# Performance work log

Measured on AMD Instinct MI355X. Metric: run time of the kernel, lower is better.

The kernel has to match this reference:

```python
import jax, jax.numpy as jnp
import numpy as np

V, E, L, H, B, T = 32000, 1024, 6, 16, 4, 1024
HS = E // H
FF = 4 * E


def setup_inputs() -> dict:
    key = jax.random.key(0)
    ks = jax.random.split(key, 16)
    s = 0.02
    n = lambda k, shp: jax.random.normal(k, shp, jnp.float32) * s
    return {
        "tokens": jax.random.randint(ks[0], (B, T), 0, V),
        "tok_emb": n(ks[1], (V, E)),
        "pos_emb": n(ks[2], (T, E)),
        "Wq": n(ks[3], (L, E, E)),
        "Wk": n(ks[4], (L, E, E)),
        "Wv": n(ks[5], (L, E, E)),
        "Wo": n(ks[6], (L, E, E)),
        "ln1_g": jnp.ones((L, E), jnp.float32),
        "ln1_b": jnp.zeros((L, E), jnp.float32),
        "W1": n(ks[7], (L, E, FF)),
        "b1": jnp.zeros((L, FF), jnp.float32),
        "W2": n(ks[8], (L, FF, E)),
        "b2": jnp.zeros((L, E), jnp.float32),
        "ln2_g": jnp.ones((L, E), jnp.float32),
        "ln2_b": jnp.zeros((L, E), jnp.float32),
        "lmh_w": n(ks[9], (E, V)),
        "lmh_b": jnp.zeros((V,), jnp.float32),
    }


def _layernorm(x, g, b):
    m = jnp.mean(x, axis=-1, keepdims=True)
    v = jnp.var(x, axis=-1, keepdims=True)
    return (x - m) * jax.lax.rsqrt(v + 1e-5) * g + b


def _forward(tokens, tok_emb, pos_emb, Wq, Wk, Wv, Wo, ln1_g, ln1_b,
             W1, b1, W2, b2, ln2_g, ln2_b, lmh_w, lmh_b):
    Bb, Tt = tokens.shape
    x = tok_emb[tokens] + pos_emb[:Tt]  # [B,T,E]
    mask = jnp.tril(jnp.ones((Tt, Tt), bool))  # causal
    scale = jnp.float32(E) ** -0.5  # NOTE: original scales by emb_dim, not head_size

    def block(x, p):
        wq, wk, wv, wo, g1, be1, w1, bb1, w2, bb2, g2, be2 = p
        h = _layernorm(x, g1, be1)
        q = (h @ wq).reshape(Bb, Tt, H, HS)
        k = (h @ wk).reshape(Bb, Tt, H, HS)
        v = (h @ wv).reshape(Bb, Tt, H, HS)
        scores = jnp.einsum('bqhd,bkhd->bhqk', q, k) * scale
        scores = jnp.where(mask, scores, -jnp.inf)
        w = jax.nn.softmax(scores, axis=-1)
        attn = jnp.einsum('bhqk,bkhd->bqhd', w, v).reshape(Bb, Tt, E)
        x = x + attn @ wo
        h2 = _layernorm(x, g2, be2)
        x = x + jax.nn.relu(h2 @ w1 + bb1) @ w2 + bb2
        return x, None

    x, _ = jax.lax.scan(block, x, (Wq, Wk, Wv, Wo, ln1_g, ln1_b,
                                   W1, b1, W2, b2, ln2_g, ln2_b))
    logits = x @ lmh_w + lmh_b  # [B,T,V]
    return logits


def reference(tokens, tok_emb, pos_emb, Wq, Wk, Wv, Wo, ln1_g, ln1_b,
              W1, b1, W2, b2, ln2_g, ln2_b, lmh_w, lmh_b):
    return _forward(tokens, tok_emb, pos_emb, Wq, Wk, Wv, Wo, ln1_g, ln1_b,
                    W1, b1, W2, b2, ln2_g, ln2_b, lmh_w, lmh_b)
```

## Files before the change

### kernel.cpp

```cpp
#include <hip/hip_runtime.h>
#include <cstdint>
#include <cstddef>

typedef __bf16 bf16;
typedef __attribute__((ext_vector_type(8))) __bf16 bf16x8;
typedef __attribute__((ext_vector_type(4))) float f32x4;

constexpr int kV = 32000, kE = 1024, kL = 6, kH = 16, kB = 4, kT = 1024;
constexpr int kHS = 64, kFF = 4096;
constexpr int kM = kB * kT;
constexpr float kScale = 0.03125f;

typedef __attribute__((address_space(1))) void gv_t;
typedef __attribute__((address_space(3))) void lv_t;

__device__ inline void gload_lds16(const void* g, void* l) {
  __builtin_amdgcn_global_load_lds((gv_t*)g, (lv_t*)l, 16, 0, 0);
}

#define SB0() __builtin_amdgcn_sched_barrier(0)
#define LGK0() asm volatile("s_waitcnt lgkmcnt(0)" ::: "memory")

enum { EPI_BF16 = 0, EPI_BF16_BIAS_RELU = 1, EPI_F32 = 2, EPI_F32_RES = 3, EPI_F32_BIAS = 4 };

__device__ inline void xcd_swz(int& bx, int& by) {
  int gx = gridDim.x, gy = gridDim.y;
  int nxy = gx * gy;
  int orig = by * gx + bx;
  int q = nxy >> 3, r = nxy & 7, xcd = orig & 7, idx = orig >> 3;
  int logical = (xcd < r ? xcd * (q + 1) : r * (q + 1) + (xcd - r) * q) + idx;
  bx = logical / gy;
  by = logical % gy;
}

template <int EPI>
__global__ __launch_bounds__(512, 2) void gemm256_k(
    const bf16* __restrict__ Ag, const bf16* __restrict__ Bg, void* Cg,
    const float* __restrict__ bias, const float* __restrict__ resid,
    int K, long lda, long ldb, long ldc) {
  extern __shared__ bf16 lds[];
  constexpr int SL = 8192;
  bf16* As = lds;
  bf16* Bs = lds + 4 * SL;

  const int tid = threadIdx.x, lane = tid & 63, w = tid >> 6;
  int bx = blockIdx.x, by = blockIdx.y;
  xcd_swz(bx, by);
  const long tm = (long)by * 256, tn = (long)bx * 256;
  const int wr = w >> 2, wc = w & 3;
  const int lr = lane & 15, kg = lane >> 4;

  const int p0 = tid, p1 = 512 + tid;
  const int r0 = p0 >> 2, ls0 = (p0 & 3) ^ ((r0 >> 1) & 3);
  const int r1 = p1 >> 2, ls1 = (p1 & 3) ^ ((r1 >> 1) & 3);
  const bf16* a0 = Ag + (tm + r0) * lda + ls0 * 8;
  const bf16* a1 = Ag + (tm + r1) * lda + ls1 * 8;
  const bf16* b0 = Bg + (tn + r0) * ldb + ls0 * 8;
  const bf16* b1 = Bg + (tn + r1) * ldb + ls1 * 8;
  const int wb = w * 1024;

  auto stage = [&](int s) {
    const int slot = s & 3;
    const long k0 = (long)s * 32;
    char* Ab = (char*)As + slot * (SL * 2);
    char* Bb = (char*)Bs + slot * (SL * 2);
    gload_lds16(a0 + k0, Ab + wb);
    gload_lds16(a1 + k0, Ab + 8192 + wb);
    gload_lds16(b0 + k0, Bb + wb);
    gload_lds16(b1 + k0, Bb + 8192 + wb);
  };

  int aoff[8], boff[4];
#pragma unroll
  for (int mi = 0; mi < 8; mi++) {
    int ar = wr * 128 + mi * 16 + lr;
    aoff[mi] = ar * 64 + ((kg ^ ((ar >> 1) & 3)) << 4);
  }
#pragma unroll
  for (int ni = 0; ni < 4; ni++) {
    int br = wc * 64 + ni * 16 + lr;
    boff[ni] = br * 64 + ((kg ^ ((br >> 1) & 3)) << 4);
  }

  f32x4 acc[8][4] = {};
  stage(0);
  stage(1);
  stage(2);
  const int NS = K >> 5;
  for (int s = 0; s < NS; s++) {
    SB0();
    if (s <= NS - 3)
      asm volatile("s_waitcnt vmcnt(8)" ::: "memory");
    else if (s == NS - 2)
      asm volatile("s_waitcnt vmcnt(4)" ::: "memory");
    else
      asm volatile("s_waitcnt vmcnt(0)" ::: "memory");
    __builtin_amdgcn_s_barrier();
    SB0();
    if (s + 3 < NS) stage(s + 3);
    const char* Ab = (const char*)As + (s & 3) * (SL * 2);
    const char* Bb = (const char*)Bs + (s & 3) * (SL * 2);
    bf16x8 af[8], bfr[4];
#pragma unroll
    for (int mi = 0; mi < 8; mi++) af[mi] = *(const bf16x8*)(Ab + aoff[mi]);
#pragma unroll
    for (int ni = 0; ni < 4; ni++) bfr[ni] = *(const bf16x8*)(Bb + boff[ni]);
    __builtin_amdgcn_s_setprio(1);
#pragma unroll
    for (int mi = 0; mi < 8; mi++)
#pragma unroll
      for (int ni = 0; ni < 4; ni++)
        acc[mi][ni] =
            __builtin_amdgcn_mfma_f32_16x16x32_bf16(af[mi], bfr[ni], acc[mi][ni], 0, 0, 0);
    __builtin_amdgcn_s_setprio(0);
  }

#pragma unroll
  for (int mi = 0; mi < 8; mi++) {
#pragma unroll
    for (int ni = 0; ni < 4; ni++) {
      const long rr = tm + wr * 128 + mi * 16 + kg * 4;
      const long cc = tn + wc * 64 + ni * 16 + lr;
      float bi = 0.f;
      if constexpr (EPI == EPI_BF16_BIAS_RELU || EPI == EPI_F32_BIAS) bi = bias[cc];
      if constexpr (EPI == EPI_F32_RES) bi = bias ? bias[cc] : 0.f;
#pragma unroll
      for (int j = 0; j < 4; j++) {
        long off = (rr + j) * ldc + cc;
        float val = acc[mi][ni][j];
        if constexpr (EPI == EPI_BF16)
          ((bf16*)Cg)[off] = (bf16)val;
        else if constexpr (EPI == EPI_BF16_BIAS_RELU)
          ((bf16*)Cg)[off] = (bf16)fmaxf(val + bi, 0.f);
        else if constexpr (EPI == EPI_F32)
          ((float*)Cg)[off] = val;
        else if constexpr (EPI == EPI_F32_RES)
          ((float*)Cg)[off] = resid[off] + val + bi;
        else
          ((float*)Cg)[off] = val + bi;
      }
    }
  }
}

template <int EPI>
__global__ __launch_bounds__(256, 2) void ring128_k(
    const bf16* __restrict__ Ag, const bf16* __restrict__ Bg, void* Cg,
    const float* __restrict__ bias, const float* __restrict__ resid,
    int K, long lda, long ldb, long ldc) {
  extern __shared__ bf16 lds[];
  char* Lb = (char*)lds;
  const int tid = threadIdx.x, lane = tid & 63, w = tid >> 6;
  int bx = blockIdx.x, by = blockIdx.y;
  xcd_swz(bx, by);
  const long tm = (long)by * 128, tn = (long)bx * 128;
  const int wr = w >> 1, wc = w & 1;
  const int lr = lane & 15, kg = lane >> 4;

  const int r0 = tid >> 2, g0 = (tid & 3) ^ ((r0 >> 1) & 3);
  const int r1 = (256 + tid) >> 2, g1 = ((256 + tid) & 3) ^ ((r1 >> 1) & 3);
  const bf16* a0 = Ag + (tm + r0) * lda + g0 * 8;
  const bf16* a1 = Ag + (tm + r1) * lda + g1 * 8;
  const bf16* b0 = Bg + (tn + r0) * ldb + g0 * 8;
  const bf16* b1 = Bg + (tn + r1) * ldb + g1 * 8;
  const int wb = w * 1024;

  auto stage = [&](int s) {
    const int slot = s & 3;
    const long k0 = (long)s * 32;
    char* Ab = Lb + slot * 16384;
    char* Bb = Ab + 8192;
    gload_lds16(a0 + k0, Ab + wb);
    gload_lds16(a1 + k0, Ab + 4096 + wb);
    gload_lds16(b0 + k0, Bb + wb);
    gload_lds16(b1 + k0, Bb + 4096 + wb);
  };

  int aoff[4], boff[4];
#pragma unroll
  for (int mi = 0; mi < 4; mi++) {
    int ar = wr * 64 + mi * 16 + lr;
    aoff[mi] = ar * 64 + ((kg ^ ((ar >> 1) & 3)) << 4);
  }
#pragma unroll
  for (int ni = 0; ni < 4; ni++) {
    int br = wc * 64 + ni * 16 + lr;
    boff[ni] = br * 64 + ((kg ^ ((br >> 1) & 3)) << 4);
  }

  f32x4 acc[4][4] = {};
  stage(0);
  stage(1);
  stage(2);
  const int NS = K >> 5;
  for (int s = 0; s < NS; s++) {
    SB0();
    if (s <= NS - 3)
      asm volatile("s_waitcnt vmcnt(8)" ::: "memory");
    else if (s == NS - 2)
      asm volatile("s_waitcnt vmcnt(4)" ::: "memory");
    else
      asm volatile("s_waitcnt vmcnt(0)" ::: "memory");
    __builtin_amdgcn_s_barrier();
    SB0();
    if (s + 3 < NS) stage(s + 3);
    const char* Ab = Lb + (s & 3) * 16384;
    const char* Bb = Ab + 8192;
    bf16x8 af[4], bfr[4];
#pragma unroll
    for (int mi = 0; mi < 4; mi++) af[mi] = *(const bf16x8*)(Ab + aoff[mi]);
#pragma unroll
    for (int ni = 0; ni < 4; ni++) bfr[ni] = *(const bf16x8*)(Bb + boff[ni]);
    __builtin_amdgcn_s_setprio(1);
#pragma unroll
    for (int mi = 0; mi < 4; mi++)
#pragma unroll
      for (int ni = 0; ni < 4; ni++)
        acc[mi][ni] =
            __builtin_amdgcn_mfma_f32_16x16x32_bf16(af[mi], bfr[ni], acc[mi][ni], 0, 0, 0);
    __builtin_amdgcn_s_setprio(0);
  }

#pragma unroll
  for (int mi = 0; mi < 4; mi++) {
#pragma unroll
    for (int ni = 0; ni < 4; ni++) {
      const long rr = tm + wr * 64 + mi * 16 + kg * 4;
      const long cc = tn + wc * 64 + ni * 16 + lr;
      float bi = 0.f;
      if constexpr (EPI == EPI_BF16_BIAS_RELU || EPI == EPI_F32_BIAS) bi = bias[cc];
      if constexpr (EPI == EPI_F32_RES) bi = bias ? bias[cc] : 0.f;
#pragma unroll
      for (int j = 0; j < 4; j++) {
        long off = (rr + j) * ldc + cc;
        float val = acc[mi][ni][j];
        if constexpr (EPI == EPI_BF16)
          ((bf16*)Cg)[off] = (bf16)val;
        else if constexpr (EPI == EPI_BF16_BIAS_RELU)
          ((bf16*)Cg)[off] = (bf16)fmaxf(val + bi, 0.f);
        else if constexpr (EPI == EPI_F32)
          ((float*)Cg)[off] = val;
        else if constexpr (EPI == EPI_F32_RES)
          ((float*)Cg)[off] = resid[off] + val + bi;
        else
          ((float*)Cg)[off] = val + bi;
      }
    }
  }
}

template <int BM, int BN, int WM, int WN, int EPI, bool CAUSAL>
__global__ __launch_bounds__((BM / WM) * (BN / WN) * 64) void gemm_k(
    const bf16* __restrict__ Ag, const bf16* __restrict__ Bg, void* Cg,
    const float* __restrict__ bias, const float* resid, int K, long lda, long ldb,
    long ldc, long sA1, long sA2, long sB1, long sB2, long sC1, long sC2, int zdiv) {
  constexpr int BK = 32;
  constexpr int NWM = BM / WM, NWN = BN / WN, NW = NWM * NWN, THREADS = NW * 64;
  constexpr int MI = WM / 16, NI = WN / 16;
  constexpr int A_CH = (BM * BK * 2) / (THREADS * 16);
  constexpr int B_CH = (BN * BK * 2) / (THREADS * 16);
  static_assert(A_CH >= 1 && B_CH >= 1, "staging chunks");
  __shared__ bf16 As[2][BM * BK];
  __shared__ bf16 Bs[2][BN * BK];
  const int tid = threadIdx.x, lane = tid & 63;
  int bx = blockIdx.x, by = blockIdx.y;
  const int z = blockIdx.z;
  if (gridDim.z == 1) xcd_swz(bx, by);
  const long tm = (long)by * BM, tn = (long)bx * BN;
  if (CAUSAL && tn > tm + (BM - 1)) return;
  const int zq = z / zdiv, zr = z % zdiv;
  Ag += (long)zq * sA1 + (long)zr * sA2;
  Bg += (long)zq * sB1 + (long)zr * sB2;
  const long cbase = (long)zq * sC1 + (long)zr * sC2;
  const int w = tid >> 6;
  const int wr = w / NWN, wc = w % NWN;
  const int wm0 = wr * WM, wn0 = wc * WN;
  const int lr = lane & 15, kg = lane >> 4;
  f32x4 acc[MI][NI] = {};

  auto stage = [&](int buf, int k0) {
#pragma unroll
    for (int i = 0; i < A_CH; i++) {
      int qq = i * THREADS + tid;
      gload_lds16(Ag + (tm + (qq >> 2)) * lda + k0 + (qq & 3) * 8,
                  (char*)&As[buf][0] + (i * THREADS + (tid & ~63)) * 16);
    }
#pragma unroll
    for (int i = 0; i < B_CH; i++) {
      int qq = i * THREADS + tid;
      gload_lds16(Bg + (tn + (qq >> 2)) * ldb + k0 + (qq & 3) * 8,
                  (char*)&Bs[buf][0] + (i * THREADS + (tid & ~63)) * 16);
    }
  };

  const int nt = K / BK;
  stage(0, 0);
  __syncthreads();
  int cur = 0;
  for (int t = 0; t < nt; t++) {
    if (t + 1 < nt) stage(cur ^ 1, (t + 1) * BK);
    bf16x8 af[MI], bfr[NI];
#pragma unroll
    for (int mi = 0; mi < MI; mi++)
      af[mi] = *(const bf16x8*)&As[cur][(wm0 + mi * 16 + lr) * BK + kg * 8];
#pragma unroll
    for (int ni = 0; ni < NI; ni++)
      bfr[ni] = *(const bf16x8*)&Bs[cur][(wn0 + ni * 16 + lr) * BK + kg * 8];
#pragma unroll
    for (int mi = 0; mi < MI; mi++)
#pragma unroll
      for (int ni = 0; ni < NI; ni++)
        acc[mi][ni] =
            __builtin_amdgcn_mfma_f32_16x16x32_bf16(af[mi], bfr[ni], acc[mi][ni], 0, 0, 0);
    __syncthreads();
    cur ^= 1;
  }

#pragma unroll
  for (int mi = 0; mi < MI; mi++) {
#pragma unroll
    for (int ni = 0; ni < NI; ni++) {
      const long rr = tm + wm0 + mi * 16 + kg * 4;
      const long cc = tn + wn0 + ni * 16 + lr;
      float bi = 0.f;
      if constexpr (EPI == EPI_BF16_BIAS_RELU || EPI == EPI_F32_BIAS) bi = bias[cc];
      if constexpr (EPI == EPI_F32_RES) bi = bias ? bias[cc] : 0.f;
#pragma unroll
      for (int j = 0; j < 4; j++) {
        long off = cbase + (rr + j) * ldc + cc;
        float val = acc[mi][ni][j];
        if constexpr (EPI == EPI_BF16)
          ((bf16*)Cg)[off] = (bf16)val;
        else if constexpr (EPI == EPI_BF16_BIAS_RELU)
          ((bf16*)Cg)[off] = (bf16)fmaxf(val + bi, 0.f);
        else if constexpr (EPI == EPI_F32)
          ((float*)Cg)[off] = val;
        else if constexpr (EPI == EPI_F32_RES)
          ((float*)Cg)[off] = resid[off] + val + bi;
        else
          ((float*)Cg)[off] = val + bi;
      }
    }
  }
}

__global__ __launch_bounds__(256, 2) void fa_k(const bf16* __restrict__ qkv,
                                               bf16* __restrict__ out) {
  extern __shared__ bf16 lds[];
  char* L = (char*)lds;
  const int tid = threadIdx.x, lane = tid & 63, wq = tid >> 6;
  const int lr = lane & 15, kg = lane >> 4;
  const int pair = blockIdx.x, z = blockIdx.y;
  const int b = z >> 4, hh = z & 15;
  const long bq = (long)b * kT;

  auto stageKV = [&](int buf, int t) {
    const bf16* kb = qkv + (bq + t * 64) * 3072 + 1024 + hh * 64;
#pragma unroll
    for (int i = 0; i < 2; i++) {
      int p = i * 256 + tid;
      int key = p >> 3, s = p & 7;
      gload_lds16(kb + (long)key * 3072 + ((s ^ (key & 7)) * 8),
                  L + 16384 + buf * 8192 + (i * 256 + (tid & ~63)) * 16);
      gload_lds16(kb + (long)key * 3072 + 1024 + s * 8,
                  L + 32768 + buf * 8192 + (i * 256 + (tid & ~63)) * 16);
    }
  };
  char* Pw = L + 58368 + wq * 4608;

  for (int sidx = 0; sidx < 2; sidx++) {
    const int qt = sidx ? 7 - pair : pair;
    const int q0 = qt * 128;
    const bf16* qbase = qkv + (bq + q0) * 3072 + hh * 64;

#pragma unroll
    for (int i = 0; i < 4; i++) {
      int p = i * 256 + tid;
      int row = p >> 3, s = p & 7;
      gload_lds16(qbase + (long)row * 3072 + ((s ^ (row & 7)) * 8),
                  L + (i * 256 + (tid & ~63)) * 16);
    }
    stageKV(0, 0);
    __syncthreads();

    bf16x8 qf[2][2];
#pragma unroll
    for (int mi = 0; mi < 2; mi++)
#pragma unroll
      for (int ks = 0; ks < 2; ks++) {
        int qr = wq * 32 + mi * 16 + lr;
        qf[mi][ks] = *(const bf16x8*)(L + qr * 128 + ((ks * 64 + kg * 16) ^ ((qr & 7) << 4)));
      }

    f32x4 O[2][4] = {};
    float mrun[2][4], lrun[2][4];
#pragma unroll
    for (int mi = 0; mi < 2; mi++)
#pragma unroll
      for (int j = 0; j < 4; j++) {
        mrun[mi][j] = -3e38f;
        lrun[mi][j] = 0.f;
      }

    const int nt = 2 * qt + 2;
    int cur = 0;
    for (int t = 0; t < nt; t++) {
      if (t + 1 < nt) stageKV(cur ^ 1, t + 1);
      {
        const char* Vb = L + 32768 + cur * 8192;
        char* VTb = L + 49152;
#pragma unroll
        for (int i = 0; i < 2; i++) {
          int p = i * 256 + tid;
          int key = p >> 3, s = p & 7;
          bf16x8 vv = *(const bf16x8*)(Vb + p * 16);
#pragma unroll
          for (int e = 0; e < 8; e++)
            *(bf16*)(VTb + (s * 8 + e) * 144 + ((key * 2) ^ (s << 4))) = vv[e];
        }
      }
      LGK0();
      SB0();
      __builtin_amdgcn_s_barrier();
      SB0();

      const char* Kb = L + 16384 + cur * 8192;
      f32x4 S[2][4] = {};
#pragma unroll
      for (int ks = 0; ks < 2; ks++) {
        bf16x8 kf[4];
#pragma unroll
        for (int ni = 0; ni < 4; ni++) {
          int key = ni * 16 + lr;
          kf[ni] = *(const bf16x8*)(Kb + key * 128 + ((ks * 64 + kg * 16) ^ ((key & 7) << 4)));
        }
#pragma unroll
        for (int mi = 0; mi < 2; mi++)
#pragma unroll
          for (int ni = 0; ni < 4; ni++)
            S[mi][ni] =
                __builtin_amdgcn_mfma_f32_16x16x32_bf16(qf[mi][ks], kf[ni], S[mi][ni], 0, 0, 0);
      }

      const int kv0 = t * 64;
#pragma unroll
      for (int mi = 0; mi < 2; mi++) {
        const int qg = q0 + wq * 32 + mi * 16 + kg * 4;
#pragma unroll
        for (int j = 0; j < 4; j++) {
          float m0 = -3e38f;
#pragma unroll
          for (int ni = 0; ni < 4; ni++) {
            float v = (kv0 + ni * 16 + lr > qg + j) ? -3e38f : S[mi][ni][j];
            S[mi][ni][j] = v;
            m0 = fmaxf(m0, v);
          }
          m0 = fmaxf(m0, __shfl_xor(m0, 1));
          m0 = fmaxf(m0, __shfl_xor(m0, 2));
          m0 = fmaxf(m0, __shfl_xor(m0, 4));
          m0 = fmaxf(m0, __shfl_xor(m0, 8));
          float mnew = fmaxf(mrun[mi][j], m0);
          float alpha = __expf((mrun[mi][j] - mnew) * kScale);
          mrun[mi][j] = mnew;
          lrun[mi][j] *= alpha;
#pragma unroll
          for (int di = 0; di < 4; di++) O[mi][di][j] *= alpha;
          float rs = 0.f;
#pragma unroll
          for (int ni = 0; ni < 4; ni++) {
            float v = S[mi][ni][j];
            float p = (v <= -1e38f) ? 0.f : __expf((v - mnew) * kScale);
            S[mi][ni][j] = p;
            rs += p;
          }
          rs += __shfl_xor(rs, 1);
          rs += __shfl_xor(rs, 2);
          rs += __shfl_xor(rs, 4);
          rs += __shfl_xor(rs, 8);
          lrun[mi][j] += rs;
        }
#pragma unroll
        for (int ni = 0; ni < 4; ni++)
#pragma unroll
          for (int j = 0; j < 4; j++)
            *(bf16*)(Pw + (mi * 16 + kg * 4 + j) * 144 + (ni * 16 + lr) * 2) =
                (bf16)S[mi][ni][j];
      }
      LGK0();
      SB0();

      const char* VTb = L + 49152;
#pragma unroll
      for (int ks = 0; ks < 2; ks++) {
        bf16x8 pf[2], vf[4];
#pragma unroll
        for (int mi = 0; mi < 2; mi++)
          pf[mi] = *(const bf16x8*)(Pw + (mi * 16 + lr) * 144 + ks * 64 + kg * 16);
#pragma unroll
        for (int di = 0; di < 4; di++) {
          int d = di * 16 + lr;
          vf[di] =
              *(const bf16x8*)(VTb + d * 144 + ((ks * 64 + kg * 16) ^ (((d >> 3) & 7) << 4)));
        }
#pragma unroll
        for (int mi = 0; mi < 2; mi++)
#pragma unroll
          for (int di = 0; di < 4; di++)
            O[mi][di] =
                __builtin_amdgcn_mfma_f32_16x16x32_bf16(pf[mi], vf[di], O[mi][di], 0, 0, 0);
      }
      __syncthreads();
      cur ^= 1;
    }

#pragma unroll
    for (int mi = 0; mi < 2; mi++)
#pragma unroll
      for (int j = 0; j < 4; j++) {
        float inv = 1.f / lrun[mi][j];
        long grow = bq + q0 + wq * 32 + mi * 16 + kg * 4 + j;
#pragma unroll
        for (int di = 0; di < 4; di++)
          out[grow * kE + hh * 64 + di * 16 + lr] = (bf16)(O[mi][di][j] * inv);
      }
  }
}

__global__ void tcvt_k(const float* __restrict__ in, bf16* __restrict__ out, int K, int N,
                       long in_zs, long out_zs) {
  __shared__ float t[32][33];
  long z = blockIdx.z;
  in += z * in_zs;
  out += z * out_zs;
  int n0 = blockIdx.x * 32, k0 = blockIdx.y * 32;
  int tx = threadIdx.x, ty = threadIdx.y;
#pragma unroll
  for (int i = 0; i < 32; i += 8) t[ty + i][tx] = in[(long)(k0 + ty + i) * N + n0 + tx];
  __syncthreads();
#pragma unroll
  for (int i = 0; i < 32; i += 8)
    out[(long)(n0 + ty + i) * K + k0 + tx] = (bf16)t[tx][ty + i];
}

__global__ void embed_k(const int* __restrict__ toks, const float* __restrict__ te,
                        const float* __restrict__ pe, float* __restrict__ x) {
  int row = blockIdx.x, tid = threadIdx.x;
  int t = row & (kT - 1);
  long tok = toks[row];
  float4 a = ((const float4*)(te + tok * kE))[tid];
  float4 p = ((const float4*)(pe + (long)t * kE))[tid];
  float4 r{a.x + p.x, a.y + p.y, a.z + p.z, a.w + p.w};
  ((float4*)(x + (long)row * kE))[tid] = r;
}

__global__ void ln_k(const float* __restrict__ x, const float* __restrict__ g,
                     const float* __restrict__ b, bf16* __restrict__ h) {
  int row = blockIdx.x, tid = threadIdx.x, lane = tid & 63, w = tid >> 6;
  const float4 v = ((const float4*)(x + (long)row * kE))[tid];
  float s = v.x + v.y + v.z + v.w;
  float ss = v.x * v.x + v.y * v.y + v.z * v.z + v.w * v.w;
#pragma unroll
  for (int o = 32; o; o >>= 1) {
    s += __shfl_xor(s, o);
    ss += __shfl_xor(ss, o);
  }
  __shared__ float r1[4], r2[4];
  if (lane == 0) { r1[w] = s; r2[w] = ss; }
  __syncthreads();
  s = r1[0] + r1[1] + r1[2] + r1[3];
  ss = r2[0] + r2[1] + r2[2] + r2[3];
  float mean = s * (1.f / kE);
  float var = ss * (1.f / kE) - mean * mean;
  float rs = rsqrtf(var + 1e-5f);
  float4 gg = ((const float4*)g)[tid];
  float4 bb = ((const float4*)b)[tid];
  union { bf16 o[4]; uint2 u; } pk;
  pk.o[0] = (bf16)((v.x - mean) * rs * gg.x + bb.x);
  pk.o[1] = (bf16)((v.y - mean) * rs * gg.y + bb.y);
  pk.o[2] = (bf16)((v.z - mean) * rs * gg.z + bb.z);
  pk.o[3] = (bf16)((v.w - mean) * rs * gg.w + bb.w);
  ((uint2*)(h + (long)row * kE))[tid] = pk.u;
}

__global__ void cast_k(const float* __restrict__ x, bf16* __restrict__ o) {
  long i = (long)blockIdx.x * 256 + threadIdx.x;
  float4 v = ((const float4*)x)[i];
  union { bf16 b[4]; uint2 u; } pk;
  pk.b[0] = (bf16)v.x;
  pk.b[1] = (bf16)v.y;
  pk.b[2] = (bf16)v.z;
  pk.b[3] = (bf16)v.w;
  ((uint2*)o)[i] = pk.u;
}

extern "C" void kernel_launch(void* const* d_in, const int* in_sizes, int n_in,
                              void* d_out, int out_size, void* d_ws, size_t ws_size,
                              hipStream_t stream) {
  const int* toks = (const int*)d_in[0];
  const float* te = (const float*)d_in[1];
  const float* pe = (const float*)d_in[2];
  const float* Wq = (const float*)d_in[3];
  const float* Wk = (const float*)d_in[4];
  const float* Wv = (const float*)d_in[5];
  const float* Wo = (const float*)d_in[6];
  const float* g1 = (const float*)d_in[7];
  const float* be1 = (const float*)d_in[8];
  const float* W1 = (const float*)d_in[9];
  const float* bb1 = (const float*)d_in[10];
  const float* W2 = (const float*)d_in[11];
  const float* bb2 = (const float*)d_in[12];
  const float* g2 = (const float*)d_in[13];
  const float* be2 = (const float*)d_in[14];
  const float* lmw = (const float*)d_in[15];
  const float* lmb = (const float*)d_in[16];

  hipFuncSetAttribute(reinterpret_cast<const void*>(&gemm256_k<EPI_BF16>),
                      hipFuncAttributeMaxDynamicSharedMemorySize, 131072);
  hipFuncSetAttribute(reinterpret_cast<const void*>(&gemm256_k<EPI_BF16_BIAS_RELU>),
                      hipFuncAttributeMaxDynamicSharedMemorySize, 131072);
  hipFuncSetAttribute(reinterpret_cast<const void*>(&gemm256_k<EPI_F32_BIAS>),
                      hipFuncAttributeMaxDynamicSharedMemorySize, 131072);
  hipFuncSetAttribute(reinterpret_cast<const void*>(&ring128_k<EPI_F32_RES>),
                      hipFuncAttributeMaxDynamicSharedMemorySize, 65536);
  hipFuncSetAttribute(reinterpret_cast<const void*>(&fa_k),
                      hipFuncAttributeMaxDynamicSharedMemorySize, 76800);

  char* ws = (char*)d_ws;
  size_t off = 0;
  auto alloc = [&](size_t bytes) -> char* {
    char* p = ws + off;
    off += (bytes + 255) & ~(size_t)255;
    return p;
  };
  bf16* WqkvT = (bf16*)alloc((size_t)kL * 3 * kE * kE * 2);
  bf16* WoT = (bf16*)alloc((size_t)kL * kE * kE * 2);
  bf16* W1T = (bf16*)alloc((size_t)kL * kE * kFF * 2);
  bf16* W2T = (bf16*)alloc((size_t)kL * kE * kFF * 2);
  bf16* lmT = (bf16*)alloc((size_t)kV * kE * 2);
  float* x = (float*)alloc((size_t)kM * kE * 4);
  bf16* h = (bf16*)alloc((size_t)kM * kE * 2);
  bf16* qkv = (bf16*)alloc((size_t)kM * 3 * kE * 2);
  bf16* at = (bf16*)alloc((size_t)kM * kE * 2);

  bf16* mid = (bf16*)d_out;

  const long EE = (long)kE * kE;
  dim3 tb(32, 8);
  tcvt_k<<<dim3(kE / 32, kE / 32, kL), tb, 0, stream>>>(Wq, WqkvT, kE, kE, EE, 3 * EE);
  tcvt_k<<<dim3(kE / 32, kE / 32, kL), tb, 0, stream>>>(Wk, WqkvT + EE, kE, kE, EE, 3 * EE);
  tcvt_k<<<dim3(kE / 32, kE / 32, kL), tb, 0, stream>>>(Wv, WqkvT + 2 * EE, kE, kE, EE, 3 * EE);
  tcvt_k<<<dim3(kE / 32, kE / 32, kL), tb, 0, stream>>>(Wo, WoT, kE, kE, EE, EE);
  tcvt_k<<<dim3(kFF / 32, kE / 32, kL), tb, 0, stream>>>(W1, W1T, kE, kFF, 4 * EE, 4 * EE);
  tcvt_k<<<dim3(kE / 32, kFF / 32, kL), tb, 0, stream>>>(W2, W2T, kFF, kE, 4 * EE, 4 * EE);
  tcvt_k<<<dim3(kV / 32, kE / 32, 1), tb, 0, stream>>>(lmw, lmT, kE, kV, 0, 0);

  embed_k<<<kM, 256, 0, stream>>>(toks, te, pe, x);

  for (int l = 0; l < kL; l++) {
    ln_k<<<kM, 256, 0, stream>>>(x, g1 + l * kE, be1 + l * kE, h);
    gemm256_k<EPI_BF16><<<dim3(3 * kE / 256, kM / 256), 512, 131072, stream>>>(
        h, WqkvT + (size_t)l * 3 * EE, qkv, nullptr, nullptr, kE, kE, kE, 3 * kE);
    fa_k<<<dim3(4, kB * kH), 256, 76800, stream>>>(qkv, at);
    gemm_k<128, 128, 64, 64, EPI_F32_RES, false><<<dim3(kE / 128, kM / 128, 1), 256, 0, stream>>>(
        at, WoT + (size_t)l * EE, x, nullptr, x, kE, kE, kE, kE, 0, 0, 0, 0, 0, 0, 1);
    ln_k<<<kM, 256, 0, stream>>>(x, g2 + l * kE, be2 + l * kE, h);
    gemm256_k<EPI_BF16_BIAS_RELU><<<dim3(kFF / 256, kM / 256), 512, 131072, stream>>>(
        h, W1T + (size_t)l * (size_t)kFF * kE, mid, bb1 + l * kFF, nullptr, kE, kE, kE, kFF);
    ring128_k<EPI_F32_RES><<<dim3(kE / 128, kM / 128), 256, 65536, stream>>>(
        mid, W2T + (size_t)l * (size_t)kE * kFF, x, bb2 + l * kE, x, kFF, kFF, kFF, kE);
  }
  cast_k<<<kM * kE / 1024, 256, 0, stream>>>(x, h);
  gemm256_k<EPI_F32_BIAS><<<dim3(kV / 256, kM / 256), 512, 131072, stream>>>(
      h, lmT, d_out, lmb, nullptr, kE, kE, kE, kV);
}
```

Before: 2.122 ms.

## Pre-transpose V globally and split flash-attention grid per query tile

```diff
diff --git a/kernel.cpp b/kernel.cpp
--- a/kernel.cpp
+++ b/kernel.cpp
@@ -249,280 +249,186 @@
   }
 }
 
-template <int BM, int BN, int WM, int WN, int EPI, bool CAUSAL>
-__global__ __launch_bounds__((BM / WM) * (BN / WN) * 64) void gemm_k(
-    const bf16* __restrict__ Ag, const bf16* __restrict__ Bg, void* Cg,
-    const float* __restrict__ bias, const float* resid, int K, long lda, long ldb,
-    long ldc, long sA1, long sA2, long sB1, long sB2, long sC1, long sC2, int zdiv) {
-  constexpr int BK = 32;
-  constexpr int NWM = BM / WM, NWN = BN / WN, NW = NWM * NWN, THREADS = NW * 64;
-  constexpr int MI = WM / 16, NI = WN / 16;
-  constexpr int A_CH = (BM * BK * 2) / (THREADS * 16);
-  constexpr int B_CH = (BN * BK * 2) / (THREADS * 16);
-  static_assert(A_CH >= 1 && B_CH >= 1, "staging chunks");
-  __shared__ bf16 As[2][BM * BK];
-  __shared__ bf16 Bs[2][BN * BK];
-  const int tid = threadIdx.x, lane = tid & 63;
-  int bx = blockIdx.x, by = blockIdx.y;
-  const int z = blockIdx.z;
-  if (gridDim.z == 1) xcd_swz(bx, by);
-  const long tm = (long)by * BM, tn = (long)bx * BN;
-  if (CAUSAL && tn > tm + (BM - 1)) return;
-  const int zq = z / zdiv, zr = z % zdiv;
-  Ag += (long)zq * sA1 + (long)zr * sA2;
-  Bg += (long)zq * sB1 + (long)zr * sB2;
-  const long cbase = (long)zq * sC1 + (long)zr * sC2;
-  const int w = tid >> 6;
-  const int wr = w / NWN, wc = w % NWN;
-  const int wm0 = wr * WM, wn0 = wc * WN;
-  const int lr = lane & 15, kg = lane >> 4;
-  f32x4 acc[MI][NI] = {};
-
-  auto stage = [&](int buf, int k0) {
-#pragma unroll
-    for (int i = 0; i < A_CH; i++) {
-      int qq = i * THREADS + tid;
-      gload_lds16(Ag + (tm + (qq >> 2)) * lda + k0 + (qq & 3) * 8,
-                  (char*)&As[buf][0] + (i * THREADS + (tid & ~63)) * 16);
-    }
-#pragma unroll
-    for (int i = 0; i < B_CH; i++) {
-      int qq = i * THREADS + tid;
-      gload_lds16(Bg + (tn + (qq >> 2)) * ldb + k0 + (qq & 3) * 8,
-                  (char*)&Bs[buf][0] + (i * THREADS + (tid & ~63)) * 16);
-    }
-  };
-
-  const int nt = K / BK;
-  stage(0, 0);
-  __syncthreads();
-  int cur = 0;
-  for (int t = 0; t < nt; t++) {
-    if (t + 1 < nt) stage(cur ^ 1, (t + 1) * BK);
-    bf16x8 af[MI], bfr[NI];
-#pragma unroll
-    for (int mi = 0; mi < MI; mi++)
-      af[mi] = *(const bf16x8*)&As[cur][(wm0 + mi * 16 + lr) * BK + kg * 8];
-#pragma unroll
-    for (int ni = 0; ni < NI; ni++)
-      bfr[ni] = *(const bf16x8*)&Bs[cur][(wn0 + ni * 16 + lr) * BK + kg * 8];
-#pragma unroll
-    for (int mi = 0; mi < MI; mi++)
-#pragma unroll
-      for (int ni = 0; ni < NI; ni++)
-        acc[mi][ni] =
-            __builtin_amdgcn_mfma_f32_16x16x32_bf16(af[mi], bfr[ni], acc[mi][ni], 0, 0, 0);
-    __syncthreads();
-    cur ^= 1;
-  }
-
-#pragma unroll
-  for (int mi = 0; mi < MI; mi++) {
-#pragma unroll
-    for (int ni = 0; ni < NI; ni++) {
-      const long rr = tm + wm0 + mi * 16 + kg * 4;
-      const long cc = tn + wn0 + ni * 16 + lr;
-      float bi = 0.f;
-      if constexpr (EPI == EPI_BF16_BIAS_RELU || EPI == EPI_F32_BIAS) bi = bias[cc];
-      if constexpr (EPI == EPI_F32_RES) bi = bias ? bias[cc] : 0.f;
-#pragma unroll
-      for (int j = 0; j < 4; j++) {
-        long off = cbase + (rr + j) * ldc + cc;
-        float val = acc[mi][ni][j];
-        if constexpr (EPI == EPI_BF16)
-          ((bf16*)Cg)[off] = (bf16)val;
-        else if constexpr (EPI == EPI_BF16_BIAS_RELU)
-          ((bf16*)Cg)[off] = (bf16)fmaxf(val + bi, 0.f);
-        else if constexpr (EPI == EPI_F32)
-          ((float*)Cg)[off] = val;
-        else if constexpr (EPI == EPI_F32_RES)
-          ((float*)Cg)[off] = resid[off] + val + bi;
-        else
-          ((float*)Cg)[off] = val + bi;
-      }
-    }
-  }
-}
-
 __global__ __launch_bounds__(256, 2) void fa_k(const bf16* __restrict__ qkv,
+                                               const bf16* __restrict__ vtG,
                                                bf16* __restrict__ out) {
   extern __shared__ bf16 lds[];
   char* L = (char*)lds;
   const int tid = threadIdx.x, lane = tid & 63, wq = tid >> 6;
   const int lr = lane & 15, kg = lane >> 4;
-  const int pair = blockIdx.x, z = blockIdx.y;
-  const int b = z >> 4, hh = z & 15;
+  const int bh = blockIdx.x, z = blockIdx.y;
+  const int b = bh >> 4, hh = bh & 15;
   const long bq = (long)b * kT;
-
+  const int qt = z < 4 ? z : 11 - z;
+  const int q0 = qt * 128;
+  const bf16* qbase = qkv + (bq + q0) * 3072 + hh * 64;
+  const bf16* vbase = vtG + (long)bh * 64 * kT;
+
+#pragma unroll
+  for (int i = 0; i < 4; i++) {
+    int p = i * 256 + tid;
+    int row = p >> 3, s = p & 7;
+    gload_lds16(qbase + (long)row * 3072 + ((s ^ (row & 7)) * 8),
+                L + (i * 256 + (tid & ~63)) * 16);
+  }
   auto stageKV = [&](int buf, int t) {
     const bf16* kb = qkv + (bq + t * 64) * 3072 + 1024 + hh * 64;
+    const bf16* vb = vbase + t * 64;
 #pragma unroll
     for (int i = 0; i < 2; i++) {
       int p = i * 256 + tid;
       int key = p >> 3, s = p & 7;
       gload_lds16(kb + (long)key * 3072 + ((s ^ (key & 7)) * 8),
                   L + 16384 + buf * 8192 + (i * 256 + (tid & ~63)) * 16);
-      gload_lds16(kb + (long)key * 3072 + 1024 + s * 8,
+      gload_lds16(vb + (long)key * kT + s * 8,
                   L + 32768 + buf * 8192 + (i * 256 + (tid & ~63)) * 16);
     }
   };
-  char* Pw = L + 58368 + wq * 4608;
-
-  for (int sidx = 0; sidx < 2; sidx++) {
-    const int qt = sidx ? 7 - pair : pair;
-    const int q0 = qt * 128;
-    const bf16* qbase = qkv + (bq + q0) * 3072 + hh * 64;
-
-#pragma unroll
-    for (int i = 0; i < 4; i++) {
-      int p = i * 256 + tid;
-      int row = p >> 3, s = p & 7;
-      gload_lds16(qbase + (long)row * 3072 + ((s ^ (row & 7)) * 8),
-                  L + (i * 256 + (tid & ~63)) * 16);
-    }
-    stageKV(0, 0);
+  stageKV(0, 0);
+  __syncthreads();
+
+  bf16x8 qf[2][2];
+#pragma unroll
+  for (int mi = 0; mi < 2; mi++)
+#pragma unroll
+    for (int ks = 0; ks < 2; ks++) {
+      int qr = wq * 32 + mi * 16 + lr;
+      qf[mi][ks] = *(const bf16x8*)(L + qr * 128 + ((ks * 64 + kg * 16) ^ ((qr & 7) << 4)));
+    }
+
+  f32x4 O[2][4] = {};
+  float mrun[2][4], lrun[2][4];
+#pragma unroll
+  for (int mi = 0; mi < 2; mi++)
+#pragma unroll
+    for (int j = 0; j < 4; j++) {
+      mrun[mi][j] = -3e38f;
+      lrun[mi][j] = 0.f;
+    }
+  char* Pw = L + 49152 + wq * 4608;
+
+  const int nt = 2 * qt + 2;
+  int cur = 0;
+  for (int t = 0; t < nt; t++) {
+    if (t + 1 < nt) stageKV(cur ^ 1, t + 1);
+
+    const char* Kb = L + 16384 + cur * 8192;
+    f32x4 S[2][4] = {};
+#pragma unroll
+    for (int ks = 0; ks < 2; ks++) {
+      bf16x8 kf[4];
+#pragma unroll
+      for (int ni = 0; ni < 4; ni++) {
+        int key = ni * 16 + lr;
+        kf[ni] = *(const bf16x8*)(Kb + key * 128 + ((ks * 64 + kg * 16) ^ ((key & 7) << 4)));
+      }
+#pragma unroll
+      for (int mi = 0; mi < 2; mi++)
+#pragma unroll
+        for (int ni = 0; ni < 4; ni++)
+          S[mi][ni] =
+              __builtin_amdgcn_mfma_f32_16x16x32_bf16(qf[mi][ks], kf[ni], S[mi][ni], 0, 0, 0);
+    }
+
+    const int kv0 = t * 64;
+#pragma unroll
+    for (int mi = 0; mi < 2; mi++) {
+      const int qg = q0 + wq * 32 + mi * 16 + kg * 4;
+#pragma unroll
+      for (int j = 0; j < 4; j++) {
+        float m0 = -3e38f;
+#pragma unroll
+        for (int ni = 0; ni < 4; ni++) {
+          float v = (kv0 + ni * 16 + lr > qg + j) ? -3e38f : S[mi][ni][j];
+          S[mi][ni][j] = v;
+          m0 = fmaxf(m0, v);
+        }
+        m0 = fmaxf(m0, __shfl_xor(m0, 1));
+        m0 = fmaxf(m0, __shfl_xor(m0, 2));
+        m0 = fmaxf(m0, __shfl_xor(m0, 4));
+        m0 = fmaxf(m0, __shfl_xor(m0, 8));
+        float mnew = fmaxf(mrun[mi][j], m0);
+        float alpha = __expf((mrun[mi][j] - mnew) * kScale);
+        mrun[mi][j] = mnew;
+        lrun[mi][j] *= alpha;
+#pragma unroll
+        for (int di = 0; di < 4; di++) O[mi][di][j] *= alpha;
+        float rs = 0.f;
+#pragma unroll
+        for (int ni = 0; ni < 4; ni++) {
+          float v = S[mi][ni][j];
+          float p = (v <= -1e38f) ? 0.f : __expf((v - mnew) * kScale);
+          S[mi][ni][j] = p;
+          rs += p;
+        }
+        rs += __shfl_xor(rs, 1);
+        rs += __shfl_xor(rs, 2);
+        rs += __shfl_xor(rs, 4);
+        rs += __shfl_xor(rs, 8);
+        lrun[mi][j] += rs;
+      }
+#pragma unroll
+      for (int ni = 0; ni < 4; ni++)
+#pragma unroll
+        for (int j = 0; j < 4; j++)
+          *(bf16*)(Pw + (mi * 16 + kg * 4 + j) * 144 + (ni * 16 + lr) * 2) =
+              (bf16)S[mi][ni][j];
+    }
+    LGK0();
+    SB0();
+
+    const char* Vb = L + 32768 + cur * 8192;
+#pragma unroll
+    for (int ks = 0; ks < 2; ks++) {
+      bf16x8 pf[2], vf[4];
+#pragma unroll
+      for (int mi = 0; mi < 2; mi++)
+        pf[mi] = *(const bf16x8*)(Pw + (mi * 16 + lr) * 144 + ks * 64 + kg * 16);
+#pragma unroll
+      for (int di = 0; di < 4; di++) {
+        int d = di * 16 + lr;
+        vf[di] = *(const bf16x8*)(Vb + d * 128 + ((ks * 64 + kg * 16) ^ ((d & 7) << 4)));
+      }
+#pragma unroll
+      for (int mi = 0; mi < 2; mi++)
+#pragma unroll
+        for (int di = 0; di < 4; di++)
+          O[mi][di] =
+              __builtin_amdgcn_mfma_f32_16x16x32_bf16(pf[mi], vf[di], O[mi][di], 0, 0, 0);
+    }
     __syncthreads();
-
-    bf16x8 qf[2][2];
-#pragma unroll
-    for (int mi = 0; mi < 2; mi++)
-#pragma unroll
-      for (int ks = 0; ks < 2; ks++) {
-        int qr = wq * 32 + mi * 16 + lr;
-        qf[mi][ks] = *(const bf16x8*)(L + qr * 128 + ((ks * 64 + kg * 16) ^ ((qr & 7) << 4)));
-      }
-
-    f32x4 O[2][4] = {};
-    float mrun[2][4], lrun[2][4];
-#pragma unroll
-    for (int mi = 0; mi < 2; mi++)
-#pragma unroll
-      for (int j = 0; j < 4; j++) {
-        mrun[mi][j] = -3e38f;
-        lrun[mi][j] = 0.f;
-      }
-
-    const int nt = 2 * qt + 2;
-    int cur = 0;
-    for (int t = 0; t < nt; t++) {
-      if (t + 1 < nt) stageKV(cur ^ 1, t + 1);
-      {
-        const char* Vb = L + 32768 + cur * 8192;
-        char* VTb = L + 49152;
-#pragma unroll
-        for (int i = 0; i < 2; i++) {
-          int p = i * 256 + tid;
-          int key = p >> 3, s = p & 7;
-          bf16x8 vv = *(const bf16x8*)(Vb + p * 16);
-#pragma unroll
-          for (int e = 0; e < 8; e++)
-            *(bf16*)(VTb + (s * 8 + e) * 144 + ((key * 2) ^ (s << 4))) = vv[e];
-        }
-      }
-      LGK0();
-      SB0();
-      __builtin_amdgcn_s_barrier();
-      SB0();
-
-      const char* Kb = L + 16384 + cur * 8192;
-      f32x4 S[2][4] = {};
-#pragma unroll
-      for (int ks = 0; ks < 2; ks++) {
-        bf16x8 kf[4];
-#pragma unroll
-        for (int ni = 0; ni < 4; ni++) {
-          int key = ni * 16 + lr;
-          kf[ni] = *(const bf16x8*)(Kb + key * 128 + ((ks * 64 + kg * 16) ^ ((key & 7) << 4)));
-        }
-#pragma unroll
-        for (int mi = 0; mi < 2; mi++)
-#pragma unroll
-          for (int ni = 0; ni < 4; ni++)
-            S[mi][ni] =
-                __builtin_amdgcn_mfma_f32_16x16x32_bf16(qf[mi][ks], kf[ni], S[mi][ni], 0, 0, 0);
-      }
-
-      const int kv0 = t * 64;
-#pragma unroll
-      for (int mi = 0; mi < 2; mi++) {
-        const int qg = q0 + wq * 32 + mi * 16 + kg * 4;
-#pragma unroll
-        for (int j = 0; j < 4; j++) {
-          float m0 = -3e38f;
-#pragma unroll
-          for (int ni = 0; ni < 4; ni++) {
-            float v = (kv0 + ni * 16 + lr > qg + j) ? -3e38f : S[mi][ni][j];
-            S[mi][ni][j] = v;
-            m0 = fmaxf(m0, v);
-          }
-          m0 = fmaxf(m0, __shfl_xor(m0, 1));
-          m0 = fmaxf(m0, __shfl_xor(m0, 2));
-          m0 = fmaxf(m0, __shfl_xor(m0, 4));
-          m0 = fmaxf(m0, __shfl_xor(m0, 8));
-          float mnew = fmaxf(mrun[mi][j], m0);
-          float alpha = __expf((mrun[mi][j] - mnew) * kScale);
-          mrun[mi][j] = mnew;
-          lrun[mi][j] *= alpha;
-#pragma unroll
-          for (int di = 0; di < 4; di++) O[mi][di][j] *= alpha;
-          float rs = 0.f;
-#pragma unroll
-          for (int ni = 0; ni < 4; ni++) {
-            float v = S[mi][ni][j];
-            float p = (v <= -1e38f) ? 0.f : __expf((v - mnew) * kScale);
-            S[mi][ni][j] = p;
-            rs += p;
-          }
-          rs += __shfl_xor(rs, 1);
-          rs += __shfl_xor(rs, 2);
-          rs += __shfl_xor(rs, 4);
-          rs += __shfl_xor(rs, 8);
-          lrun[mi][j] += rs;
-        }
-#pragma unroll
-        for (int ni = 0; ni < 4; ni++)
-#pragma unroll
-          for (int j = 0; j < 4; j++)
-            *(bf16*)(Pw + (mi * 16 + kg * 4 + j) * 144 + (ni * 16 + lr) * 2) =
-                (bf16)S[mi][ni][j];
-      }
-      LGK0();
-      SB0();
-
-      const char* VTb = L + 49152;
-#pragma unroll
-      for (int ks = 0; ks < 2; ks++) {
-        bf16x8 pf[2], vf[4];
-#pragma unroll
-        for (int mi = 0; mi < 2; mi++)
-          pf[mi] = *(const bf16x8*)(Pw + (mi * 16 + lr) * 144 + ks * 64 + kg * 16);
-#pragma unroll
-        for (int di = 0; di < 4; di++) {
-          int d = di * 16 + lr;
-          vf[di] =
-              *(const bf16x8*)(VTb + d * 144 + ((ks * 64 + kg * 16) ^ (((d >> 3) & 7) << 4)));
-        }
-#pragma unroll
-        for (int mi = 0; mi < 2; mi++)
-#pragma unroll
-          for (int di = 0; di < 4; di++)
-            O[mi][di] =
-                __builtin_amdgcn_mfma_f32_16x16x32_bf16(pf[mi], vf[di], O[mi][di], 0, 0, 0);
-      }
-      __syncthreads();
-      cur ^= 1;
-    }
-
-#pragma unroll
-    for (int mi = 0; mi < 2; mi++)
-#pragma unroll
-      for (int j = 0; j < 4; j++) {
-        float inv = 1.f / lrun[mi][j];
-        long grow = bq + q0 + wq * 32 + mi * 16 + kg * 4 + j;
-#pragma unroll
-        for (int di = 0; di < 4; di++)
-          out[grow * kE + hh * 64 + di * 16 + lr] = (bf16)(O[mi][di][j] * inv);
-      }
+    cur ^= 1;
+  }
+
+#pragma unroll
+  for (int mi = 0; mi < 2; mi++)
+#pragma unroll
+    for (int j = 0; j < 4; j++) {
+      float inv = 1.f / lrun[mi][j];
+      long grow = bq + q0 + wq * 32 + mi * 16 + kg * 4 + j;
+#pragma unroll
+      for (int di = 0; di < 4; di++)
+        out[grow * kE + hh * 64 + di * 16 + lr] = (bf16)(O[mi][di][j] * inv);
+    }
+}
+
+__global__ void vtrans_k(const bf16* __restrict__ qkv, bf16* __restrict__ vt) {
+  __shared__ bf16 tbuf[32][33];
+  int z = blockIdx.z;
+  int b = z >> 4, h = z & 15;
+  int t0 = blockIdx.x * 32, s0 = blockIdx.y * 32;
+  int tx = threadIdx.x, ty = threadIdx.y;
+#pragma unroll
+  for (int i = 0; i < 32; i += 8)
+    tbuf[ty + i][tx] = qkv[((long)b * kT + t0 + ty + i) * 3072 + 2048 + h * 64 + s0 + tx];
+  __syncthreads();
+#pragma unroll
+  for (int i = 0; i < 32; i += 8) {
+    int d = s0 + ty + i;
+    int tt = t0 + tx;
+    int g = (tt >> 3) & 7, e = tt & 7;
+    long idx = ((long)z * 64 + d) * kT + (tt & ~63) + ((g ^ (d & 7)) << 3) + e;
+    vt[idx] = tbuf[tx][ty + i];
   }
 }
 
@@ -623,7 +529,7 @@
   hipFuncSetAttribute(reinterpret_cast<const void*>(&ring128_k<EPI_F32_RES>),
                       hipFuncAttributeMaxDynamicSharedMemorySize, 65536);
   hipFuncSetAttribute(reinterpret_cast<const void*>(&fa_k),
-                      hipFuncAttributeMaxDynamicSharedMemorySize, 76800);
+                      hipFuncAttributeMaxDynamicSharedMemorySize, 67584);
 
   char* ws = (char*)d_ws;
   size_t off = 0;
@@ -641,6 +547,7 @@
   bf16* h = (bf16*)alloc((size_t)kM * kE * 2);
   bf16* qkv = (bf16*)alloc((size_t)kM * 3 * kE * 2);
   bf16* at = (bf16*)alloc((size_t)kM * kE * 2);
+  bf16* vtG = (bf16*)alloc((size_t)kB * kH * 64 * kT * 2);
 
   bf16* mid = (bf16*)d_out;
 
@@ -660,9 +567,10 @@
     ln_k<<<kM, 256, 0, stream>>>(x, g1 + l * kE, be1 + l * kE, h);
     gemm256_k<EPI_BF16><<<dim3(3 * kE / 256, kM / 256), 512, 131072, stream>>>(
         h, WqkvT + (size_t)l * 3 * EE, qkv, nullptr, nullptr, kE, kE, kE, 3 * kE);
-    fa_k<<<dim3(4, kB * kH), 256, 76800, stream>>>(qkv, at);
-    gemm_k<128, 128, 64, 64, EPI_F32_RES, false><<<dim3(kE / 128, kM / 128, 1), 256, 0, stream>>>(
-        at, WoT + (size_t)l * EE, x, nullptr, x, kE, kE, kE, kE, 0, 0, 0, 0, 0, 0, 1);
+    vtrans_k<<<dim3(kT / 32, kHS / 32, kB * kH), tb, 0, stream>>>(qkv, vtG);
+    fa_k<<<dim3(kB * kH, 8), 256, 67584, stream>>>(qkv, vtG, at);
+    ring128_k<EPI_F32_RES><<<dim3(kE / 128, kM / 128), 256, 65536, stream>>>(
+        at, WoT + (size_t)l * EE, x, nullptr, x, kE, kE, kE, kE);
     ln_k<<<kM, 256, 0, stream>>>(x, g2 + l * kE, be2 + l * kE, h);
     gemm256_k<EPI_BF16_BIAS_RELU><<<dim3(kFF / 256, kM / 256), 512, 131072, stream>>>(
         h, W1T + (size_t)l * (size_t)kFF * kE, mid, bb1 + l * kFF, nullptr, kE, kE, kE, kFF);
```

Result: faster. 2.037 ms (-4.0%).
